# Kernel optimization log

Hardware: AMD Instinct MI355X
Metric: run time of the kernel (lower is better)

## Reference

```python
import jax, jax.numpy as jnp
import numpy as np

N = 100000      # nodes
E = 1600000     # edges (avg degree 16)
NF = 1          # node_feature_dim
EF = 1          # edge_feature_dim
H = 64          # hidden_dim
L = 5           # num_layers


def _linear_init(key, fan_in, fan_out):
    # torch nn.Linear default: U(-1/sqrt(fan_in), 1/sqrt(fan_in)) for W and b
    s = 1.0 / np.sqrt(fan_in)
    kw, kb = jax.random.split(key)
    w = jax.random.uniform(kw, (fan_in, fan_out), minval=-s, maxval=s, dtype=jnp.float32)
    b = jax.random.uniform(kb, (fan_out,), minval=-s, maxval=s, dtype=jnp.float32)
    return w, b


def setup_inputs() -> dict:
    key = jax.random.key(0)
    ks = jax.random.split(key, 8)
    x = jax.random.normal(ks[0], (N, NF), dtype=jnp.float32)
    edge_index = jax.random.randint(ks[1], (2, E), 0, N, dtype=jnp.int32)
    edge_attr = jax.random.uniform(ks[2], (E, EF), dtype=jnp.float32)

    emb_w, emb_b = _linear_init(ks[3], NF, H)
    fc_w, fc_b = _linear_init(ks[4], H, 1)

    msg_w1, msg_b1, msg_w2, msg_b2 = [], [], [], []
    upd_w1, upd_b1, upd_w2, upd_b2 = [], [], [], []
    lk = jax.random.split(ks[5], L)
    for l in range(L):
        k1, k2, k3, k4 = jax.random.split(lk[l], 4)
        w, b = _linear_init(k1, H + EF, H); msg_w1.append(w); msg_b1.append(b)
        w, b = _linear_init(k2, H, H);      msg_w2.append(w); msg_b2.append(b)
        w, b = _linear_init(k3, 2 * H, H);  upd_w1.append(w); upd_b1.append(b)
        w, b = _linear_init(k4, H, H);      upd_w2.append(w); upd_b2.append(b)

    stack = lambda xs: jnp.stack(xs, axis=0)
    return {
        "x": x, "edge_index": edge_index, "edge_attr": edge_attr,
        "emb_w": emb_w, "emb_b": emb_b,
        "msg_w1": stack(msg_w1), "msg_b1": stack(msg_b1),
        "msg_w2": stack(msg_w2), "msg_b2": stack(msg_b2),
        "upd_w1": stack(upd_w1), "upd_b1": stack(upd_b1),
        "upd_w2": stack(upd_w2), "upd_b2": stack(upd_b2),
        "fc_w": fc_w, "fc_b": fc_b,
    }


def reference(x, edge_index, edge_attr, emb_w, emb_b,
              msg_w1, msg_b1, msg_w2, msg_b2,
              upd_w1, upd_b1, upd_w2, upd_b2, fc_w, fc_b):
    src = edge_index[0]  # x_j (source)
    dst = edge_index[1]  # aggregation target i
    n = x.shape[0]

    h = x @ emb_w + emb_b  # [N, H]
    for l in range(msg_w1.shape[0]):
        # message: MLP(cat[x_j, edge_attr])
        m = jnp.concatenate([h[src], edge_attr], axis=1)  # [E, H+EF]
        m = jax.nn.relu(m @ msg_w1[l] + msg_b1[l]) @ msg_w2[l] + msg_b2[l]  # [E, H]
        # scatter-min aggregate; torch_scatter fills empty segments with 0
        aggr = jax.ops.segment_min(m, dst, num_segments=n)
        aggr = jnp.where(jnp.isfinite(aggr), aggr, jnp.zeros_like(aggr))
        # update: MLP(cat[x, aggr])
        u = jnp.concatenate([h, aggr], axis=1)  # [N, 2H]
        h = jax.nn.relu(u @ upd_w1[l] + upd_b1[l]) @ upd_w2[l] + upd_b2[l]
    return (h @ fc_w + fc_b).squeeze(-1)  # [N]
```

## Files before the change

kernel.cpp:

```cpp
#include <hip/hip_runtime.h>
#include <math.h>

#define N_NODES 100000
#define N_EDGES 1600000
#define HDIM 64
#define NBUCK 64
#define SCAN_T 1024
#define SCAN_CHUNK 98


__global__ __launch_bounds__(256) void k_zero_int(int* __restrict__ p, int n) {
  int i = blockIdx.x * 256 + threadIdx.x;
  if (i < n) p[i] = 0;
}

__global__ __launch_bounds__(256) void k_deg_count(const int* __restrict__ ei,
                                                   int* __restrict__ deg) {
  int e = blockIdx.x * 256 + threadIdx.x;
  if (e < N_EDGES) atomicAdd(&deg[ei[N_EDGES + e]], 1);
}

__global__ __launch_bounds__(SCAN_T) void k_rowptr(const int* __restrict__ deg,
                                                   int* __restrict__ row_ptr) {
  __shared__ int sums[SCAN_T];
  const int t = threadIdx.x;
  const int lo = t * SCAN_CHUNK;
  const int hi = min(lo + SCAN_CHUNK, N_NODES);
  int s = 0;
  for (int i = lo; i < hi; ++i) s += deg[i];
  sums[t] = s;
  __syncthreads();
  for (int off = 1; off < SCAN_T; off <<= 1) {
    int v = (t >= off) ? sums[t - off] : 0;
    __syncthreads();
    sums[t] += v;
    __syncthreads();
  }
  int run = (t == 0) ? 0 : sums[t - 1];
  for (int i = lo; i < hi; ++i) { row_ptr[i] = run; run += deg[i]; }
  if (t == SCAN_T - 1) row_ptr[N_NODES] = run;
}

__global__ __launch_bounds__(256) void k_scatter(
    const int* __restrict__ ei, const float* __restrict__ eattr,
    const int* __restrict__ row_ptr, int* __restrict__ cursor,
    int* __restrict__ s_src, float* __restrict__ s_ea) {
  int e = blockIdx.x * 256 + threadIdx.x;
  if (e >= N_EDGES) return;
  int d = ei[N_EDGES + e];
  int pos = row_ptr[d] + atomicAdd(&cursor[d], 1);
  s_src[pos] = ei[e];
  s_ea[pos] = eattr[e];
}

__global__ __launch_bounds__(256) void k_bucket_hist(const int* __restrict__ deg,
                                                     int* __restrict__ bhist) {
  int i = blockIdx.x * 256 + threadIdx.x;
  if (i < N_NODES) atomicAdd(&bhist[min(deg[i], NBUCK - 1)], 1);
}

__global__ __launch_bounds__(64) void k_bucket_scan(const int* __restrict__ bhist,
                                                    int* __restrict__ bcursor) {
  if (threadIdx.x == 0) {
    int run = 0;
    for (int b = 0; b < NBUCK; ++b) { bcursor[b] = run; run += bhist[b]; }
  }
}

__global__ __launch_bounds__(256) void k_bucket_scatter(const int* __restrict__ deg,
                                                        int* __restrict__ bcursor,
                                                        int* __restrict__ node_order) {
  __shared__ int lhist[NBUCK];
  __shared__ int lbase[NBUCK];
  __shared__ int lcur[NBUCK];
  const int t = threadIdx.x;
  const int i = blockIdx.x * 256 + t;
  if (t < NBUCK) { lhist[t] = 0; lcur[t] = 0; }
  __syncthreads();
  int b = -1;
  if (i < N_NODES) { b = min(deg[i], NBUCK - 1); atomicAdd(&lhist[b], 1); }
  __syncthreads();
  if (t < NBUCK && lhist[t] > 0) lbase[t] = atomicAdd(&bcursor[t], lhist[t]);
  __syncthreads();
  if (i < N_NODES) {
    int r = atomicAdd(&lcur[b], 1);
    node_order[lbase[b] + r] = i;
  }
}


__global__ __launch_bounds__(256) void k_embed_z(
    const float* __restrict__ x, const float* __restrict__ emb_w,
    const float* __restrict__ emb_b,
    const float* __restrict__ w1, const float* __restrict__ b1,
    float* __restrict__ h, float* __restrict__ z) {
  __shared__ float hs[64][65];
  const int t = threadIdx.x;
  const int nl = t >> 2;
  const int l4 = t & 3;
  const int i = blockIdx.x * 64 + nl;
  const bool valid = (i < N_NODES);
  const int jbase = l4 * 16;
  const float xv = valid ? x[i] : 0.0f;

  float hv[16];
  #pragma unroll
  for (int jj = 0; jj < 16; ++jj) {
    int j = jbase + jj;
    hv[jj] = fmaf(xv, emb_w[j], emb_b[j]);
    hs[nl][j] = hv[jj];
  }
  if (valid) {
    #pragma unroll
    for (int q = 0; q < 4; ++q)
      reinterpret_cast<float4*>(h + (size_t)i * HDIM)[l4 * 4 + q] =
          make_float4(hv[4*q], hv[4*q+1], hv[4*q+2], hv[4*q+3]);
  }
  __syncthreads();

  float acc[16];
  #pragma unroll
  for (int jj = 0; jj < 16; ++jj) acc[jj] = b1[jbase + jj];
  #pragma unroll 8
  for (int k = 0; k < 64; ++k) {
    float hk = hs[nl][k];
    const float* wr = w1 + k * 64 + jbase;
    #pragma unroll
    for (int jj = 0; jj < 16; ++jj) acc[jj] = fmaf(hk, wr[jj], acc[jj]);
  }
  if (valid) {
    #pragma unroll
    for (int q = 0; q < 4; ++q)
      reinterpret_cast<float4*>(z + (size_t)i * HDIM)[l4 * 4 + q] =
          make_float4(acc[4*q], acc[4*q+1], acc[4*q+2], acc[4*q+3]);
  }
}

__global__ __launch_bounds__(256) void k_aggr2(
    const int* __restrict__ node_order, const int* __restrict__ row_ptr,
    const int* __restrict__ s_src, const float* __restrict__ s_ea,
    const float* __restrict__ z,
    const float* __restrict__ w1b, const float* __restrict__ w2,
    const float* __restrict__ b2,
    float* __restrict__ aggr) {
  const int t = threadIdx.x;
  const int lane = t & 63;
  const int wv = t >> 6;
  const int half = __builtin_amdgcn_readfirstlane(wv & 1);
  const int pair = __builtin_amdgcn_readfirstlane(wv >> 1);
  const int jb = half * 32;
  const int r = blockIdx.x * 128 + pair * 64 + lane;
  if (r >= N_NODES) return;
  const int node = node_order[r];
  const int p0 = row_ptr[node];
  const int p1 = row_ptr[node + 1];

  float mn[32];
  #pragma unroll
  for (int j = 0; j < 32; ++j) mn[j] = INFINITY;

  for (int p = p0; p < p1; ++p) {
    const int src = s_src[p];
    const float ea = s_ea[p];
    const float4* zr = reinterpret_cast<const float4*>(z + (size_t)src * HDIM);

    float m[32];
    #pragma unroll
    for (int j = 0; j < 32; ++j) m[j] = b2[jb + j];

    for (int k4 = 0; k4 < 16; ++k4) {
      float4 zv = zr[k4];
      float h0 = fmaxf(fmaf(ea, w1b[4*k4+0], zv.x), 0.0f);
      float h1 = fmaxf(fmaf(ea, w1b[4*k4+1], zv.y), 0.0f);
      float h2 = fmaxf(fmaf(ea, w1b[4*k4+2], zv.z), 0.0f);
      float h3 = fmaxf(fmaf(ea, w1b[4*k4+3], zv.w), 0.0f);
      const float* wr0 = w2 + (4*k4+0) * 64 + jb;
      const float* wr1 = w2 + (4*k4+1) * 64 + jb;
      const float* wr2 = w2 + (4*k4+2) * 64 + jb;
      const float* wr3 = w2 + (4*k4+3) * 64 + jb;
      #pragma unroll
      for (int j = 0; j < 32; ++j) m[j] = fmaf(h0, wr0[j], m[j]);
      #pragma unroll
      for (int j = 0; j < 32; ++j) m[j] = fmaf(h1, wr1[j], m[j]);
      #pragma unroll
      for (int j = 0; j < 32; ++j) m[j] = fmaf(h2, wr2[j], m[j]);
      #pragma unroll
      for (int j = 0; j < 32; ++j) m[j] = fmaf(h3, wr3[j], m[j]);
    }
    #pragma unroll
    for (int j = 0; j < 32; ++j) mn[j] = fminf(mn[j], m[j]);
  }

  float4* ar = reinterpret_cast<float4*>(aggr + (size_t)node * HDIM + jb);
  #pragma unroll
  for (int q = 0; q < 8; ++q) {
    float4 v;
    v.x = isinf(mn[4*q+0]) ? 0.0f : mn[4*q+0];
    v.y = isinf(mn[4*q+1]) ? 0.0f : mn[4*q+1];
    v.z = isinf(mn[4*q+2]) ? 0.0f : mn[4*q+2];
    v.w = isinf(mn[4*q+3]) ? 0.0f : mn[4*q+3];
    ar[q] = v;
  }
}

template <int LAST>
__global__ __launch_bounds__(256) void k_update2(
    const float* __restrict__ aggr,
    const float* __restrict__ u1w, const float* __restrict__ u1b,
    const float* __restrict__ u2w, const float* __restrict__ u2b,
    const float* __restrict__ w1next, const float* __restrict__ b1next,
    const float* __restrict__ fcw, const float* __restrict__ fcb,
    float* __restrict__ h, float* __restrict__ z, float* __restrict__ out) {
  __shared__ float h1s[128][65];
  const int t = threadIdx.x;
  const int lane = t & 63;
  const int wv = t >> 6;
  const int half = __builtin_amdgcn_readfirstlane(wv & 1);
  const int pair = __builtin_amdgcn_readfirstlane(wv >> 1);
  const int jb = half * 32;
  const int nl = pair * 64 + lane;
  const int node = blockIdx.x * 128 + nl;
  const bool valid = (node < N_NODES);
  const size_t off = (size_t)(valid ? node : 0) * HDIM;

  float acc[32];
  #pragma unroll
  for (int j = 0; j < 32; ++j) acc[j] = u1b[jb + j];
  {
    const float4* hr = reinterpret_cast<const float4*>(h + off);
    for (int k4 = 0; k4 < 16; ++k4) {
      float4 uv = hr[k4];
      const float* w0 = u1w + (4*k4+0) * 64 + jb;
      const float* w1 = u1w + (4*k4+1) * 64 + jb;
      const float* w2 = u1w + (4*k4+2) * 64 + jb;
      const float* w3 = u1w + (4*k4+3) * 64 + jb;
      #pragma unroll
      for (int j = 0; j < 32; ++j) acc[j] = fmaf(uv.x, w0[j], acc[j]);
      #pragma unroll
      for (int j = 0; j < 32; ++j) acc[j] = fmaf(uv.y, w1[j], acc[j]);
      #pragma unroll
      for (int j = 0; j < 32; ++j) acc[j] = fmaf(uv.z, w2[j], acc[j]);
      #pragma unroll
      for (int j = 0; j < 32; ++j) acc[j] = fmaf(uv.w, w3[j], acc[j]);
    }
    const float4* ar = reinterpret_cast<const float4*>(aggr + off);
    for (int k4 = 0; k4 < 16; ++k4) {
      float4 uv = ar[k4];
      const float* w0 = u1w + (64 + 4*k4+0) * 64 + jb;
      const float* w1 = u1w + (64 + 4*k4+1) * 64 + jb;
      const float* w2 = u1w + (64 + 4*k4+2) * 64 + jb;
      const float* w3 = u1w + (64 + 4*k4+3) * 64 + jb;
      #pragma unroll
      for (int j = 0; j < 32; ++j) acc[j] = fmaf(uv.x, w0[j], acc[j]);
      #pragma unroll
      for (int j = 0; j < 32; ++j) acc[j] = fmaf(uv.y, w1[j], acc[j]);
      #pragma unroll
      for (int j = 0; j < 32; ++j) acc[j] = fmaf(uv.z, w2[j], acc[j]);
      #pragma unroll
      for (int j = 0; j < 32; ++j) acc[j] = fmaf(uv.w, w3[j], acc[j]);
    }
  }
  #pragma unroll
  for (int j = 0; j < 32; ++j) h1s[nl][jb + j] = fmaxf(acc[j], 0.0f);
  __syncthreads();

  float hn[32];
  #pragma unroll
  for (int j = 0; j < 32; ++j) hn[j] = u2b[jb + j];
  for (int k = 0; k < 64; ++k) {
    float hk = h1s[nl][k];
    const float* wr = u2w + k * 64 + jb;
    #pragma unroll
    for (int j = 0; j < 32; ++j) hn[j] = fmaf(hk, wr[j], hn[j]);
  }
  if (valid) {
    #pragma unroll
    for (int q = 0; q < 8; ++q)
      reinterpret_cast<float4*>(h + off)[half * 8 + q] =
          make_float4(hn[4*q], hn[4*q+1], hn[4*q+2], hn[4*q+3]);
  }

  if (LAST) {
    float s = 0.0f;
    #pragma unroll
    for (int j = 0; j < 32; ++j) s = fmaf(hn[j], fcw[jb + j], s);
    __syncthreads();
    if (half) h1s[nl][64] = s;
    __syncthreads();
    if (!half && valid) out[node] = s + h1s[nl][64] + fcb[0];
  } else {
    __syncthreads();
    #pragma unroll
    for (int j = 0; j < 32; ++j) h1s[nl][jb + j] = hn[j];
    __syncthreads();
    float zz[32];
    #pragma unroll
    for (int j = 0; j < 32; ++j) zz[j] = b1next[jb + j];
    for (int k = 0; k < 64; ++k) {
      float hk = h1s[nl][k];
      const float* wr = w1next + k * 64 + jb;
      #pragma unroll
      for (int j = 0; j < 32; ++j) zz[j] = fmaf(hk, wr[j], zz[j]);
    }
    if (valid) {
      #pragma unroll
      for (int q = 0; q < 8; ++q)
        reinterpret_cast<float4*>(z + off)[half * 8 + q] =
            make_float4(zz[4*q], zz[4*q+1], zz[4*q+2], zz[4*q+3]);
    }
  }
}

extern "C" void kernel_launch(void* const* d_in, const int* in_sizes, int n_in,
                              void* d_out, int out_size, void* d_ws, size_t ws_size,
                              hipStream_t stream) {
  const float* x      = (const float*)d_in[0];
  const int*   ei     = (const int*)d_in[1];
  const float* eattr  = (const float*)d_in[2];
  const float* emb_w  = (const float*)d_in[3];
  const float* emb_b  = (const float*)d_in[4];
  const float* msg_w1 = (const float*)d_in[5];
  const float* msg_b1 = (const float*)d_in[6];
  const float* msg_w2 = (const float*)d_in[7];
  const float* msg_b2 = (const float*)d_in[8];
  const float* upd_w1 = (const float*)d_in[9];
  const float* upd_b1 = (const float*)d_in[10];
  const float* upd_w2 = (const float*)d_in[11];
  const float* upd_b2 = (const float*)d_in[12];
  const float* fc_w   = (const float*)d_in[13];
  const float* fc_b   = (const float*)d_in[14];
  float* out = (float*)d_out;

  float* h     = (float*)d_ws;
  float* zbuf  = h + (size_t)N_NODES * HDIM;
  float* aggr  = zbuf + (size_t)N_NODES * HDIM;
  float* s_ea  = aggr + (size_t)N_NODES * HDIM;
  int*   s_src = (int*)(s_ea + N_EDGES);
  int*   row_ptr = s_src + N_EDGES;
  int*   node_order = row_ptr + (N_NODES + 1);
  int*   deg   = node_order + N_NODES;
  int*   cursor= deg + N_NODES;
  int*   bhist = cursor + N_NODES;
  int*   bcursor = bhist + NBUCK;

  const int nodeBlocks64 = (N_NODES + 63) / 64;
  const int nodeBlocks128 = (N_NODES + 127) / 128;
  const int nodeBlocks256 = (N_NODES + 255) / 256;
  const int edgeBlocks = (N_EDGES + 255) / 256;
  const int zeroN = 2 * N_NODES + NBUCK;

  k_zero_int<<<(zeroN + 255) / 256, 256, 0, stream>>>(deg, zeroN);
  k_deg_count<<<edgeBlocks, 256, 0, stream>>>(ei, deg);
  k_rowptr<<<1, SCAN_T, 0, stream>>>(deg, row_ptr);
  k_scatter<<<edgeBlocks, 256, 0, stream>>>(ei, eattr, row_ptr, cursor, s_src, s_ea);
  k_bucket_hist<<<nodeBlocks256, 256, 0, stream>>>(deg, bhist);
  k_bucket_scan<<<1, 64, 0, stream>>>(bhist, bcursor);
  k_bucket_scatter<<<nodeBlocks256, 256, 0, stream>>>(deg, bcursor, node_order);

  k_embed_z<<<nodeBlocks64, 256, 0, stream>>>(x, emb_w, emb_b, msg_w1, msg_b1, h, zbuf);

  for (int l = 0; l < 5; ++l) {
    k_aggr2<<<nodeBlocks128, 256, 0, stream>>>(
        node_order, row_ptr, s_src, s_ea, zbuf,
        msg_w1 + l * 65 * 64 + 64 * 64,
        msg_w2 + l * 64 * 64,
        msg_b2 + l * 64,
        aggr);
    if (l < 4) {
      k_update2<0><<<nodeBlocks128, 256, 0, stream>>>(
          aggr,
          upd_w1 + l * 128 * 64, upd_b1 + l * 64,
          upd_w2 + l * 64 * 64,  upd_b2 + l * 64,
          msg_w1 + (l + 1) * 65 * 64, msg_b1 + (l + 1) * 64,
          nullptr, nullptr,
          h, zbuf, nullptr);
    } else {
      k_update2<1><<<nodeBlocks128, 256, 0, stream>>>(
          aggr,
          upd_w1 + l * 128 * 64, upd_b1 + l * 64,
          upd_w2 + l * 64 * 64,  upd_b2 + l * 64,
          nullptr, nullptr,
          fc_w, fc_b,
          h, zbuf, out);
    }
  }
}
```

Baseline: 2.565 ms.

## Prefetch next edge's z row and pair heavy/light degree chunks in aggregation

The aggregation kernel now loads the next edge's 64-float z row and edge attribute into registers while computing the current edge's message MLP, a software-pipelining step meant to hide gather latency. Each block's two wave-pairs now take node chunks from opposite ends of the degree-sorted order, so heavy and light nodes share a block and block runtimes even out. It also adds launch_bounds(256,2) and fully unrolls the k loop. The extra 64 registers for the prefetch buffer raise register pressure, which may lower occupancy or cause spills.

```diff
diff --git a/kernel.cpp b/kernel.cpp
--- a/kernel.cpp
+++ b/kernel.cpp
@@ -7,6 +7,7 @@
 #define NBUCK 64
 #define SCAN_T 1024
 #define SCAN_CHUNK 98
+#define NCHUNK 1564
 
 
 __global__ __launch_bounds__(256) void k_zero_int(int* __restrict__ p, int n) {
@@ -136,7 +137,7 @@
   }
 }
 
-__global__ __launch_bounds__(256) void k_aggr2(
+__global__ __launch_bounds__(256, 2) void k_aggr3(
     const int* __restrict__ node_order, const int* __restrict__ row_ptr,
     const int* __restrict__ s_src, const float* __restrict__ s_ea,
     const float* __restrict__ z,
@@ -149,7 +150,8 @@
   const int half = __builtin_amdgcn_readfirstlane(wv & 1);
   const int pair = __builtin_amdgcn_readfirstlane(wv >> 1);
   const int jb = half * 32;
-  const int r = blockIdx.x * 128 + pair * 64 + lane;
+  const int chunk = pair ? (NCHUNK - 1 - (int)blockIdx.x) : (int)blockIdx.x;
+  const int r = chunk * 64 + lane;
   if (r >= N_NODES) return;
   const int node = node_order[r];
   const int p0 = row_ptr[node];
@@ -159,21 +161,37 @@
   #pragma unroll
   for (int j = 0; j < 32; ++j) mn[j] = INFINITY;
 
+  float4 zb[16];
+  float eab = 0.0f;
+  if (p0 < p1) {
+    const float4* zr = reinterpret_cast<const float4*>(z + (size_t)s_src[p0] * HDIM);
+    #pragma unroll
+    for (int q = 0; q < 16; ++q) zb[q] = zr[q];
+    eab = s_ea[p0];
+  }
+
   for (int p = p0; p < p1; ++p) {
-    const int src = s_src[p];
-    const float ea = s_ea[p];
-    const float4* zr = reinterpret_cast<const float4*>(z + (size_t)src * HDIM);
+    float4 zn[16];
+    float ean = 0.0f;
+    const int pn = p + 1;
+    if (pn < p1) {
+      const float4* zr = reinterpret_cast<const float4*>(z + (size_t)s_src[pn] * HDIM);
+      #pragma unroll
+      for (int q = 0; q < 16; ++q) zn[q] = zr[q];
+      ean = s_ea[pn];
+    }
 
     float m[32];
     #pragma unroll
     for (int j = 0; j < 32; ++j) m[j] = b2[jb + j];
 
+    #pragma unroll
     for (int k4 = 0; k4 < 16; ++k4) {
-      float4 zv = zr[k4];
-      float h0 = fmaxf(fmaf(ea, w1b[4*k4+0], zv.x), 0.0f);
-      float h1 = fmaxf(fmaf(ea, w1b[4*k4+1], zv.y), 0.0f);
-      float h2 = fmaxf(fmaf(ea, w1b[4*k4+2], zv.z), 0.0f);
-      float h3 = fmaxf(fmaf(ea, w1b[4*k4+3], zv.w), 0.0f);
+      float4 zv = zb[k4];
+      float h0 = fmaxf(fmaf(eab, w1b[4*k4+0], zv.x), 0.0f);
+      float h1 = fmaxf(fmaf(eab, w1b[4*k4+1], zv.y), 0.0f);
+      float h2 = fmaxf(fmaf(eab, w1b[4*k4+2], zv.z), 0.0f);
+      float h3 = fmaxf(fmaf(eab, w1b[4*k4+3], zv.w), 0.0f);
       const float* wr0 = w2 + (4*k4+0) * 64 + jb;
       const float* wr1 = w2 + (4*k4+1) * 64 + jb;
       const float* wr2 = w2 + (4*k4+2) * 64 + jb;
@@ -189,6 +207,10 @@
     }
     #pragma unroll
     for (int j = 0; j < 32; ++j) mn[j] = fminf(mn[j], m[j]);
+
+    #pragma unroll
+    for (int q = 0; q < 16; ++q) zb[q] = zn[q];
+    eab = ean;
   }
 
   float4* ar = reinterpret_cast<float4*>(aggr + (size_t)node * HDIM + jb);
@@ -360,7 +382,7 @@
   k_embed_z<<<nodeBlocks64, 256, 0, stream>>>(x, emb_w, emb_b, msg_w1, msg_b1, h, zbuf);
 
   for (int l = 0; l < 5; ++l) {
-    k_aggr2<<<nodeBlocks128, 256, 0, stream>>>(
+    k_aggr3<<<nodeBlocks128, 256, 0, stream>>>(
         node_order, row_ptr, s_src, s_ea, zbuf,
         msg_w1 + l * 65 * 64 + 64 * 64,
         msg_w2 + l * 64 * 64,
```

After: 4.730 ms. 1.84x slower.

## Fuse edge aggregation and node update into one per-layer kernel with ping-pong z

Applied to the files above, without the earlier changes.

Merges the per-layer message/min-aggregation kernel and the update-MLP kernel into a single 512-thread kernel. The aggregated vector now goes through shared memory instead of a global aggr buffer. The z buffer is double-buffered so other blocks can still read the previous layer's z while the next one is written. Each node is split across four waves of 16 output columns instead of two of 32, which raises thread count and cuts registers per thread. Blocks run in reverse order, so the highest-degree nodes (per the degree-bucketed ordering) are scheduled first for load balance. The cost is that each z row is gathered by four waves instead of two, adding gather traffic.

```diff
diff --git a/kernel.cpp b/kernel.cpp
--- a/kernel.cpp
+++ b/kernel.cpp
@@ -7,6 +7,8 @@
 #define NBUCK 64
 #define SCAN_T 1024
 #define SCAN_CHUNK 98
+#define NPB 128
+#define LBLOCKS 782
 
 
 __global__ __launch_bounds__(256) void k_zero_int(int* __restrict__ p, int n) {
@@ -136,177 +138,151 @@
   }
 }
 
-__global__ __launch_bounds__(256) void k_aggr2(
+template <int LAST>
+__global__ __launch_bounds__(512) void k_layer(
     const int* __restrict__ node_order, const int* __restrict__ row_ptr,
     const int* __restrict__ s_src, const float* __restrict__ s_ea,
-    const float* __restrict__ z,
+    const float* __restrict__ z_in,
     const float* __restrict__ w1b, const float* __restrict__ w2,
     const float* __restrict__ b2,
-    float* __restrict__ aggr) {
-  const int t = threadIdx.x;
-  const int lane = t & 63;
-  const int wv = t >> 6;
-  const int half = __builtin_amdgcn_readfirstlane(wv & 1);
-  const int pair = __builtin_amdgcn_readfirstlane(wv >> 1);
-  const int jb = half * 32;
-  const int r = blockIdx.x * 128 + pair * 64 + lane;
-  if (r >= N_NODES) return;
-  const int node = node_order[r];
-  const int p0 = row_ptr[node];
-  const int p1 = row_ptr[node + 1];
-
-  float mn[32];
-  #pragma unroll
-  for (int j = 0; j < 32; ++j) mn[j] = INFINITY;
-
-  for (int p = p0; p < p1; ++p) {
-    const int src = s_src[p];
-    const float ea = s_ea[p];
-    const float4* zr = reinterpret_cast<const float4*>(z + (size_t)src * HDIM);
-
-    float m[32];
-    #pragma unroll
-    for (int j = 0; j < 32; ++j) m[j] = b2[jb + j];
-
-    for (int k4 = 0; k4 < 16; ++k4) {
-      float4 zv = zr[k4];
-      float h0 = fmaxf(fmaf(ea, w1b[4*k4+0], zv.x), 0.0f);
-      float h1 = fmaxf(fmaf(ea, w1b[4*k4+1], zv.y), 0.0f);
-      float h2 = fmaxf(fmaf(ea, w1b[4*k4+2], zv.z), 0.0f);
-      float h3 = fmaxf(fmaf(ea, w1b[4*k4+3], zv.w), 0.0f);
-      const float* wr0 = w2 + (4*k4+0) * 64 + jb;
-      const float* wr1 = w2 + (4*k4+1) * 64 + jb;
-      const float* wr2 = w2 + (4*k4+2) * 64 + jb;
-      const float* wr3 = w2 + (4*k4+3) * 64 + jb;
-      #pragma unroll
-      for (int j = 0; j < 32; ++j) m[j] = fmaf(h0, wr0[j], m[j]);
-      #pragma unroll
-      for (int j = 0; j < 32; ++j) m[j] = fmaf(h1, wr1[j], m[j]);
-      #pragma unroll
-      for (int j = 0; j < 32; ++j) m[j] = fmaf(h2, wr2[j], m[j]);
-      #pragma unroll
-      for (int j = 0; j < 32; ++j) m[j] = fmaf(h3, wr3[j], m[j]);
-    }
-    #pragma unroll
-    for (int j = 0; j < 32; ++j) mn[j] = fminf(mn[j], m[j]);
-  }
-
-  float4* ar = reinterpret_cast<float4*>(aggr + (size_t)node * HDIM + jb);
-  #pragma unroll
-  for (int q = 0; q < 8; ++q) {
-    float4 v;
-    v.x = isinf(mn[4*q+0]) ? 0.0f : mn[4*q+0];
-    v.y = isinf(mn[4*q+1]) ? 0.0f : mn[4*q+1];
-    v.z = isinf(mn[4*q+2]) ? 0.0f : mn[4*q+2];
-    v.w = isinf(mn[4*q+3]) ? 0.0f : mn[4*q+3];
-    ar[q] = v;
-  }
-}
-
-template <int LAST>
-__global__ __launch_bounds__(256) void k_update2(
-    const float* __restrict__ aggr,
     const float* __restrict__ u1w, const float* __restrict__ u1b,
     const float* __restrict__ u2w, const float* __restrict__ u2b,
     const float* __restrict__ w1next, const float* __restrict__ b1next,
     const float* __restrict__ fcw, const float* __restrict__ fcb,
-    float* __restrict__ h, float* __restrict__ z, float* __restrict__ out) {
-  __shared__ float h1s[128][65];
+    float* __restrict__ h, float* __restrict__ z_out, float* __restrict__ out) {
+  __shared__ float xch[NPB][65];
+  __shared__ float ps[NPB][4];
   const int t = threadIdx.x;
   const int lane = t & 63;
-  const int wv = t >> 6;
-  const int half = __builtin_amdgcn_readfirstlane(wv & 1);
-  const int pair = __builtin_amdgcn_readfirstlane(wv >> 1);
-  const int jb = half * 32;
-  const int nl = pair * 64 + lane;
-  const int node = blockIdx.x * 128 + nl;
-  const bool valid = (node < N_NODES);
-  const size_t off = (size_t)(valid ? node : 0) * HDIM;
-
-  float acc[32];
-  #pragma unroll
-  for (int j = 0; j < 32; ++j) acc[j] = u1b[jb + j];
+  const int w = t >> 6;
+  const int q  = __builtin_amdgcn_readfirstlane(w & 3);
+  const int cw = __builtin_amdgcn_readfirstlane(w >> 2);
+  const int jb = q * 16;
+  const int nl = cw * 64 + lane;
+  const int r = (LBLOCKS - 1 - (int)blockIdx.x) * NPB + nl;
+  const bool valid = (r < N_NODES);
+  const int node = valid ? node_order[r] : 0;
+  const size_t hoff = (size_t)node * HDIM;
+
+  float mn[16];
+  #pragma unroll
+  for (int j = 0; j < 16; ++j) mn[j] = INFINITY;
+
+  if (valid) {
+    const int p0 = row_ptr[node];
+    const int p1 = row_ptr[node + 1];
+    for (int p = p0; p < p1; ++p) {
+      const int src = s_src[p];
+      const float ea = s_ea[p];
+      const float4* zr = reinterpret_cast<const float4*>(z_in + (size_t)src * HDIM);
+
+      float m[16];
+      #pragma unroll
+      for (int j = 0; j < 16; ++j) m[j] = b2[jb + j];
+
+      for (int k4 = 0; k4 < 16; ++k4) {
+        float4 zv = zr[k4];
+        float h0 = fmaxf(fmaf(ea, w1b[4*k4+0], zv.x), 0.0f);
+        float h1 = fmaxf(fmaf(ea, w1b[4*k4+1], zv.y), 0.0f);
+        float h2 = fmaxf(fmaf(ea, w1b[4*k4+2], zv.z), 0.0f);
+        float h3 = fmaxf(fmaf(ea, w1b[4*k4+3], zv.w), 0.0f);
+        const float* wr0 = w2 + (4*k4+0) * 64 + jb;
+        const float* wr1 = w2 + (4*k4+1) * 64 + jb;
+        const float* wr2 = w2 + (4*k4+2) * 64 + jb;
+        const float* wr3 = w2 + (4*k4+3) * 64 + jb;
+        #pragma unroll
+        for (int j = 0; j < 16; ++j) m[j] = fmaf(h0, wr0[j], m[j]);
+        #pragma unroll
+        for (int j = 0; j < 16; ++j) m[j] = fmaf(h1, wr1[j], m[j]);
+        #pragma unroll
+        for (int j = 0; j < 16; ++j) m[j] = fmaf(h2, wr2[j], m[j]);
+        #pragma unroll
+        for (int j = 0; j < 16; ++j) m[j] = fmaf(h3, wr3[j], m[j]);
+      }
+      #pragma unroll
+      for (int j = 0; j < 16; ++j) mn[j] = fminf(mn[j], m[j]);
+    }
+  }
+  #pragma unroll
+  for (int j = 0; j < 16; ++j)
+    xch[nl][jb + j] = isinf(mn[j]) ? 0.0f : mn[j];
+  __syncthreads();
+
+  float acc[16];
+  #pragma unroll
+  for (int j = 0; j < 16; ++j) acc[j] = u1b[jb + j];
   {
-    const float4* hr = reinterpret_cast<const float4*>(h + off);
+    const float4* hr = reinterpret_cast<const float4*>(h + hoff);
     for (int k4 = 0; k4 < 16; ++k4) {
       float4 uv = hr[k4];
       const float* w0 = u1w + (4*k4+0) * 64 + jb;
       const float* w1 = u1w + (4*k4+1) * 64 + jb;
-      const float* w2 = u1w + (4*k4+2) * 64 + jb;
+      const float* w2r = u1w + (4*k4+2) * 64 + jb;
       const float* w3 = u1w + (4*k4+3) * 64 + jb;
       #pragma unroll
-      for (int j = 0; j < 32; ++j) acc[j] = fmaf(uv.x, w0[j], acc[j]);
-      #pragma unroll
-      for (int j = 0; j < 32; ++j) acc[j] = fmaf(uv.y, w1[j], acc[j]);
-      #pragma unroll
-      for (int j = 0; j < 32; ++j) acc[j] = fmaf(uv.z, w2[j], acc[j]);
-      #pragma unroll
-      for (int j = 0; j < 32; ++j) acc[j] = fmaf(uv.w, w3[j], acc[j]);
-    }
-    const float4* ar = reinterpret_cast<const float4*>(aggr + off);
-    for (int k4 = 0; k4 < 16; ++k4) {
-      float4 uv = ar[k4];
-      const float* w0 = u1w + (64 + 4*k4+0) * 64 + jb;
-      const float* w1 = u1w + (64 + 4*k4+1) * 64 + jb;
-      const float* w2 = u1w + (64 + 4*k4+2) * 64 + jb;
-      const float* w3 = u1w + (64 + 4*k4+3) * 64 + jb;
-      #pragma unroll
-      for (int j = 0; j < 32; ++j) acc[j] = fmaf(uv.x, w0[j], acc[j]);
-      #pragma unroll
-      for (int j = 0; j < 32; ++j) acc[j] = fmaf(uv.y, w1[j], acc[j]);
-      #pragma unroll
-      for (int j = 0; j < 32; ++j) acc[j] = fmaf(uv.z, w2[j], acc[j]);
-      #pragma unroll
-      for (int j = 0; j < 32; ++j) acc[j] = fmaf(uv.w, w3[j], acc[j]);
-    }
-  }
-  #pragma unroll
-  for (int j = 0; j < 32; ++j) h1s[nl][jb + j] = fmaxf(acc[j], 0.0f);
-  __syncthreads();
-
-  float hn[32];
-  #pragma unroll
-  for (int j = 0; j < 32; ++j) hn[j] = u2b[jb + j];
+      for (int j = 0; j < 16; ++j) acc[j] = fmaf(uv.x, w0[j], acc[j]);
+      #pragma unroll
+      for (int j = 0; j < 16; ++j) acc[j] = fmaf(uv.y, w1[j], acc[j]);
+      #pragma unroll
+      for (int j = 0; j < 16; ++j) acc[j] = fmaf(uv.z, w2r[j], acc[j]);
+      #pragma unroll
+      for (int j = 0; j < 16; ++j) acc[j] = fmaf(uv.w, w3[j], acc[j]);
+    }
+    for (int k = 0; k < 64; ++k) {
+      float uk = xch[nl][k];
+      const float* wr = u1w + (64 + k) * 64 + jb;
+      #pragma unroll
+      for (int j = 0; j < 16; ++j) acc[j] = fmaf(uk, wr[j], acc[j]);
+    }
+  }
+  __syncthreads();
+  #pragma unroll
+  for (int j = 0; j < 16; ++j) xch[nl][jb + j] = fmaxf(acc[j], 0.0f);
+  __syncthreads();
+
+  float hn[16];
+  #pragma unroll
+  for (int j = 0; j < 16; ++j) hn[j] = u2b[jb + j];
   for (int k = 0; k < 64; ++k) {
-    float hk = h1s[nl][k];
+    float hk = xch[nl][k];
     const float* wr = u2w + k * 64 + jb;
     #pragma unroll
-    for (int j = 0; j < 32; ++j) hn[j] = fmaf(hk, wr[j], hn[j]);
+    for (int j = 0; j < 16; ++j) hn[j] = fmaf(hk, wr[j], hn[j]);
   }
   if (valid) {
     #pragma unroll
-    for (int q = 0; q < 8; ++q)
-      reinterpret_cast<float4*>(h + off)[half * 8 + q] =
-          make_float4(hn[4*q], hn[4*q+1], hn[4*q+2], hn[4*q+3]);
+    for (int v = 0; v < 4; ++v)
+      reinterpret_cast<float4*>(h + hoff)[q * 4 + v] =
+          make_float4(hn[4*v], hn[4*v+1], hn[4*v+2], hn[4*v+3]);
   }
 
   if (LAST) {
     float s = 0.0f;
     #pragma unroll
-    for (int j = 0; j < 32; ++j) s = fmaf(hn[j], fcw[jb + j], s);
-    __syncthreads();
-    if (half) h1s[nl][64] = s;
-    __syncthreads();
-    if (!half && valid) out[node] = s + h1s[nl][64] + fcb[0];
+    for (int j = 0; j < 16; ++j) s = fmaf(hn[j], fcw[jb + j], s);
+    ps[nl][q] = s;
+    __syncthreads();
+    if (q == 0 && valid)
+      out[node] = ps[nl][0] + ps[nl][1] + ps[nl][2] + ps[nl][3] + fcb[0];
   } else {
     __syncthreads();
     #pragma unroll
-    for (int j = 0; j < 32; ++j) h1s[nl][jb + j] = hn[j];
-    __syncthreads();
-    float zz[32];
-    #pragma unroll
-    for (int j = 0; j < 32; ++j) zz[j] = b1next[jb + j];
+    for (int j = 0; j < 16; ++j) xch[nl][jb + j] = hn[j];
+    __syncthreads();
+    float zz[16];
+    #pragma unroll
+    for (int j = 0; j < 16; ++j) zz[j] = b1next[jb + j];
     for (int k = 0; k < 64; ++k) {
-      float hk = h1s[nl][k];
+      float hk = xch[nl][k];
       const float* wr = w1next + k * 64 + jb;
       #pragma unroll
-      for (int j = 0; j < 32; ++j) zz[j] = fmaf(hk, wr[j], zz[j]);
+      for (int j = 0; j < 16; ++j) zz[j] = fmaf(hk, wr[j], zz[j]);
     }
     if (valid) {
       #pragma unroll
-      for (int q = 0; q < 8; ++q)
-        reinterpret_cast<float4*>(z + off)[half * 8 + q] =
-            make_float4(zz[4*q], zz[4*q+1], zz[4*q+2], zz[4*q+3]);
+      for (int v = 0; v < 4; ++v)
+        reinterpret_cast<float4*>(z_out + hoff)[q * 4 + v] =
+            make_float4(zz[4*v], zz[4*v+1], zz[4*v+2], zz[4*v+3]);
     }
   }
 }
@@ -332,9 +308,9 @@
   float* out = (float*)d_out;
 
   float* h     = (float*)d_ws;
-  float* zbuf  = h + (size_t)N_NODES * HDIM;
-  float* aggr  = zbuf + (size_t)N_NODES * HDIM;
-  float* s_ea  = aggr + (size_t)N_NODES * HDIM;
+  float* zA    = h + (size_t)N_NODES * HDIM;
+  float* zB    = zA + (size_t)N_NODES * HDIM;
+  float* s_ea  = zB + (size_t)N_NODES * HDIM;
   int*   s_src = (int*)(s_ea + N_EDGES);
   int*   row_ptr = s_src + N_EDGES;
   int*   node_order = row_ptr + (N_NODES + 1);
@@ -344,7 +320,6 @@
   int*   bcursor = bhist + NBUCK;
 
   const int nodeBlocks64 = (N_NODES + 63) / 64;
-  const int nodeBlocks128 = (N_NODES + 127) / 128;
   const int nodeBlocks256 = (N_NODES + 255) / 256;
   const int edgeBlocks = (N_EDGES + 255) / 256;
   const int zeroN = 2 * N_NODES + NBUCK;
@@ -357,31 +332,33 @@
   k_bucket_scan<<<1, 64, 0, stream>>>(bhist, bcursor);
   k_bucket_scatter<<<nodeBlocks256, 256, 0, stream>>>(deg, bcursor, node_order);
 
-  k_embed_z<<<nodeBlocks64, 256, 0, stream>>>(x, emb_w, emb_b, msg_w1, msg_b1, h, zbuf);
-
+  k_embed_z<<<nodeBlocks64, 256, 0, stream>>>(x, emb_w, emb_b, msg_w1, msg_b1, h, zA);
+
+  float* zin = zA;
+  float* zout = zB;
   for (int l = 0; l < 5; ++l) {
-    k_aggr2<<<nodeBlocks128, 256, 0, stream>>>(
-        node_order, row_ptr, s_src, s_ea, zbuf,
-        msg_w1 + l * 65 * 64 + 64 * 64,
-        msg_w2 + l * 64 * 64,
-        msg_b2 + l * 64,
-        aggr);
+    const float* w1b = msg_w1 + l * 65 * 64 + 64 * 64;
+    const float* w2  = msg_w2 + l * 64 * 64;
+    const float* b2  = msg_b2 + l * 64;
+    const float* u1w = upd_w1 + l * 128 * 64;
+    const float* u1b = upd_b1 + l * 64;
+    const float* u2w = upd_w2 + l * 64 * 64;
+    const float* u2b = upd_b2 + l * 64;
     if (l < 4) {
-      k_update2<0><<<nodeBlocks128, 256, 0, stream>>>(
-          aggr,
-          upd_w1 + l * 128 * 64, upd_b1 + l * 64,
-          upd_w2 + l * 64 * 64,  upd_b2 + l * 64,
+      k_layer<0><<<LBLOCKS, 512, 0, stream>>>(
+          node_order, row_ptr, s_src, s_ea, zin,
+          w1b, w2, b2, u1w, u1b, u2w, u2b,
           msg_w1 + (l + 1) * 65 * 64, msg_b1 + (l + 1) * 64,
           nullptr, nullptr,
-          h, zbuf, nullptr);
+          h, zout, nullptr);
+      float* tmp = zin; zin = zout; zout = tmp;
     } else {
-      k_update2<1><<<nodeBlocks128, 256, 0, stream>>>(
-          aggr,
-          upd_w1 + l * 128 * 64, upd_b1 + l * 64,
-          upd_w2 + l * 64 * 64,  upd_b2 + l * 64,
+      k_layer<1><<<LBLOCKS, 512, 0, stream>>>(
+          node_order, row_ptr, s_src, s_ea, zin,
+          w1b, w2, b2, u1w, u1b, u2w, u2b,
           nullptr, nullptr,
           fc_w, fc_b,
-          h, zbuf, out);
-    }
-  }
-}
+          h, nullptr, out);
+    }
+  }
+}
```

Result: slower. 2.688 ms (+4.8%).
